# Optimization experiments

Measured on AMD Instinct MI355X. Metric: run time of the kernel, lower is better.

The kernel has to match this reference:

```python
import jax, jax.numpy as jnp
import numpy as np

N_NODES = 10000
N_EDGES = 320000
D_IN = 128
D_HID = 256
D_OUT = 128


def setup_inputs() -> dict:
    key = jax.random.key(0)
    k = jax.random.split(key, 6)
    idx_i = jax.random.randint(k[0], (N_EDGES,), 0, N_NODES)
    idx_j = jax.random.randint(k[1], (N_EDGES,), 0, N_NODES)
    prop = jax.random.normal(k[2], (N_NODES, D_IN), dtype=jnp.float32)
    basis = jax.random.normal(k[3], (N_EDGES, D_IN), dtype=jnp.float32)
    W1 = jax.random.normal(k[4], (D_IN, D_HID), dtype=jnp.float32) * (1.0 / np.sqrt(D_IN))
    b1 = jnp.zeros((D_HID,), dtype=jnp.float32)
    W2 = jax.random.normal(k[5], (D_HID, D_OUT), dtype=jnp.float32) * (1.0 / np.sqrt(D_HID))
    b2 = jnp.zeros((D_OUT,), dtype=jnp.float32)
    return {"idx_i": idx_i, "idx_j": idx_j, "prop": prop, "basis": basis,
            "W1": W1, "b1": b1, "W2": W2, "b2": b2}


def reference(idx_i, idx_j, prop, basis, W1, b1, W2, b2):
    # gather node features to edges, combine with basis: [E, D_IN]
    inter = prop[idx_i] + basis + prop[idx_j]
    # MLP: Linear(128->256) + tanh, then Linear(256->128) (no final activation)
    h = jnp.tanh(inter @ W1 + b1)  # [E, D_HID]
    out = h @ W2 + b2              # [E, D_OUT]
    return out
```

## Files before the change

kernel.cpp:

```cpp
#include <hip/hip_runtime.h>


#define N_EDGES 320000
#define DI 128
#define DH 256
#define DO 128
#define TM 64
#define NT_TILES (N_EDGES / TM)
#define PERSIST_GRID 768

typedef _Float16 half8v __attribute__((ext_vector_type(8)));
typedef _Float16 half4v __attribute__((ext_vector_type(4)));
typedef float floatx16 __attribute__((ext_vector_type(16)));

__device__ __forceinline__ float fast_tanh(float x) {
    float ax = __builtin_fabsf(x);
    float e = __expf(2.0f * ax);
    float t = 1.0f - 2.0f * __builtin_amdgcn_rcpf(e + 1.0f);
    return __builtin_copysignf(t, x);
}

#define BAR() do { asm volatile("s_waitcnt lgkmcnt(0)" ::: "memory"); \
                   __builtin_amdgcn_s_barrier();                      \
                   asm volatile("" ::: "memory"); } while (0)

__global__ __launch_bounds__(256) void wconvert(
    const float* __restrict__ W1, const float* __restrict__ W2,
    _Float16* __restrict__ W1T, _Float16* __restrict__ W2T)
{
    __shared__ float sT[32][33];
    int b = blockIdx.x;
    const float* src; _Float16* dst; int R, C, r0, c0;
    if (b < 32) { src = W1; dst = W1T; R = DI;  C = DH; r0 = (b & 3) * 32;  c0 = (b >> 2) * 32; }
    else { b -= 32; src = W2; dst = W2T; R = DH; C = DO; r0 = (b & 7) * 32; c0 = (b >> 3) * 32; }

    const int tid = threadIdx.x;
    const int cc = tid & 31, rr = tid >> 5;
    #pragma unroll
    for (int p = 0; p < 4; ++p) {
        int r = rr + p * 8;
        sT[r][cc] = src[(size_t)(r0 + r) * C + c0 + cc];
    }
    __syncthreads();
    #pragma unroll
    for (int p = 0; p < 4; ++p) {
        int c = rr + p * 8;
        dst[(size_t)(c0 + c) * R + r0 + cc] = (_Float16)sT[cc][c];
    }
}

__global__ __launch_bounds__(256, 2) void pilayer_main(
    const int* __restrict__ idx_i, const int* __restrict__ idx_j,
    const float* __restrict__ prop, const float* __restrict__ basis,
    const _Float16* __restrict__ W1T, const float* __restrict__ b1,
    const _Float16* __restrict__ W2T, const float* __restrict__ b2,
    float* __restrict__ out)
{
    __shared__ _Float16 sA[TM][DI + 8];
    __shared__ _Float16 sH[TM][DH + 8];

    const int tid = threadIdx.x;
    const int w   = tid >> 6;
    const int l   = tid & 63;
    const int lm  = l & 31;
    const int lk  = (l >> 5) * 8;
    const int rowq = 4 * (l >> 5);
    const int c4  = (tid & 31) * 4;
    const int r0  = tid >> 5;

    int t = blockIdx.x;

    {
        #pragma unroll
        for (int p = 0; p < 8; ++p) {
            const int r = r0 + p * 8;
            const int e = t * TM + r;
            const int ii = idx_i[e], jj = idx_j[e];
            const float4 a  = *(const float4*)(prop  + (size_t)ii * DI + c4);
            const float4 bv = *(const float4*)(prop  + (size_t)jj * DI + c4);
            const float4 c  = *(const float4*)(basis + (size_t)e  * DI + c4);
            half4v hv;
            hv[0] = (_Float16)(a.x + bv.x + c.x);
            hv[1] = (_Float16)(a.y + bv.y + c.y);
            hv[2] = (_Float16)(a.z + bv.z + c.z);
            hv[3] = (_Float16)(a.w + bv.w + c.w);
            *(half4v*)(&sA[r][c4]) = hv;
        }
    }
    BAR();

    for (; t < NT_TILES; t += PERSIST_GRID) {
        const int tn = t + PERSIST_GRID;
        const bool pf = (tn < NT_TILES);

        int ii[8], jj[8];
        float4 gc[8];
        if (pf) {
            #pragma unroll
            for (int p = 0; p < 8; ++p) {
                const int e = tn * TM + r0 + p * 8;
                ii[p] = idx_i[e];
                jj[p] = idx_j[e];
                gc[p] = *(const float4*)(basis + (size_t)e * DI + c4);
            }
        }

        floatx16 hacc[2][2] = {};
        {
            const _Float16* w1p = W1T + (size_t)(w * 64 + lm) * DI + lk;
            __builtin_amdgcn_s_setprio(1);
            #pragma unroll 4
            for (int kt = 0; kt < 8; ++kt) {
                const int ko = kt * 16;
                half8v a0  = *(const half8v*)(&sA[lm][ko + lk]);
                half8v a1  = *(const half8v*)(&sA[32 + lm][ko + lk]);
                half8v b0  = *(const half8v*)(w1p + ko);
                half8v b1f = *(const half8v*)(w1p + 32 * DI + ko);
                hacc[0][0] = __builtin_amdgcn_mfma_f32_32x32x16_f16(a0, b0,  hacc[0][0], 0, 0, 0);
                hacc[1][0] = __builtin_amdgcn_mfma_f32_32x32x16_f16(a1, b0,  hacc[1][0], 0, 0, 0);
                hacc[0][1] = __builtin_amdgcn_mfma_f32_32x32x16_f16(a0, b1f, hacc[0][1], 0, 0, 0);
                hacc[1][1] = __builtin_amdgcn_mfma_f32_32x32x16_f16(a1, b1f, hacc[1][1], 0, 0, 0);
            }
            __builtin_amdgcn_s_setprio(0);
        }

        float4 ga[8], gb[8];
        if (pf) {
            #pragma unroll
            for (int p = 0; p < 8; ++p) {
                ga[p] = *(const float4*)(prop + (size_t)ii[p] * DI + c4);
                gb[p] = *(const float4*)(prop + (size_t)jj[p] * DI + c4);
            }
        }

        {
            const float bias0 = b1[w * 64 + lm];
            const float bias1 = b1[w * 64 + 32 + lm];
            #pragma unroll
            for (int mt = 0; mt < 2; ++mt) {
                #pragma unroll
                for (int r = 0; r < 16; ++r) {
                    const int row = mt * 32 + (r & 3) + 8 * (r >> 2) + rowq;
                    sH[row][w * 64 + lm]      = (_Float16)fast_tanh(hacc[mt][0][r] + bias0);
                    sH[row][w * 64 + 32 + lm] = (_Float16)fast_tanh(hacc[mt][1][r] + bias1);
                }
            }
        }
        BAR();

        floatx16 oacc[2] = {};
        {
            const _Float16* w2p = W2T + (size_t)(w * 32 + lm) * DH + lk;
            __builtin_amdgcn_s_setprio(1);
            #pragma unroll 4
            for (int kt = 0; kt < 16; ++kt) {
                const int ko = kt * 16;
                half8v a0 = *(const half8v*)(&sH[lm][ko + lk]);
                half8v a1 = *(const half8v*)(&sH[32 + lm][ko + lk]);
                half8v bb = *(const half8v*)(w2p + ko);
                oacc[0] = __builtin_amdgcn_mfma_f32_32x32x16_f16(a0, bb, oacc[0], 0, 0, 0);
                oacc[1] = __builtin_amdgcn_mfma_f32_32x32x16_f16(a1, bb, oacc[1], 0, 0, 0);
            }
            __builtin_amdgcn_s_setprio(0);
        }

        if (pf) {
            #pragma unroll
            for (int p = 0; p < 8; ++p) {
                const int r = r0 + p * 8;
                half4v hv;
                hv[0] = (_Float16)(ga[p].x + gb[p].x + gc[p].x);
                hv[1] = (_Float16)(ga[p].y + gb[p].y + gc[p].y);
                hv[2] = (_Float16)(ga[p].z + gb[p].z + gc[p].z);
                hv[3] = (_Float16)(ga[p].w + gb[p].w + gc[p].w);
                *(half4v*)(&sA[r][c4]) = hv;
            }
        }

        {
            const int col = w * 32 + lm;
            const float bias = b2[col];
            #pragma unroll
            for (int mt = 0; mt < 2; ++mt) {
                #pragma unroll
                for (int r = 0; r < 16; ++r) {
                    const int row = t * TM + mt * 32 + (r & 3) + 8 * (r >> 2) + rowq;
                    __builtin_nontemporal_store(oacc[mt][r] + bias,
                                                out + (size_t)row * DO + col);
                }
            }
        }

        BAR();
    }
}

extern "C" void kernel_launch(void* const* d_in, const int* in_sizes, int n_in,
                              void* d_out, int out_size, void* d_ws, size_t ws_size,
                              hipStream_t stream) {
    const int*   idx_i = (const int*)d_in[0];
    const int*   idx_j = (const int*)d_in[1];
    const float* prop  = (const float*)d_in[2];
    const float* basis = (const float*)d_in[3];
    const float* W1    = (const float*)d_in[4];
    const float* b1    = (const float*)d_in[5];
    const float* W2    = (const float*)d_in[6];
    const float* b2    = (const float*)d_in[7];
    float* out = (float*)d_out;

    _Float16* W1T = (_Float16*)d_ws;
    _Float16* W2T = W1T + (size_t)DI * DH;

    wconvert<<<64, 256, 0, stream>>>(W1, W2, W1T, W2T);
    pilayer_main<<<PERSIST_GRID, 256, 0, stream>>>(idx_i, idx_j, prop, basis,
                                                   W1T, b1, W2T, b2, out);
}
```

Before: 399.6 us.

## Precompute per-node prop@W1 and gather projected features instead of raw props

```diff
diff --git a/kernel.cpp b/kernel.cpp
--- a/kernel.cpp
+++ b/kernel.cpp
@@ -2,27 +2,21 @@
 
 
 #define N_EDGES 320000
+#define N_NODES 10000
 #define DI 128
 #define DH 256
 #define DO 128
 #define TM 64
-#define NT_TILES (N_EDGES / TM)
-#define PERSIST_GRID 768
+#define NBLK (N_EDGES / TM)
 
 typedef _Float16 half8v __attribute__((ext_vector_type(8)));
 typedef _Float16 half4v __attribute__((ext_vector_type(4)));
 typedef float floatx16 __attribute__((ext_vector_type(16)));
 
 __device__ __forceinline__ float fast_tanh(float x) {
-    float ax = __builtin_fabsf(x);
-    float e = __expf(2.0f * ax);
-    float t = 1.0f - 2.0f * __builtin_amdgcn_rcpf(e + 1.0f);
-    return __builtin_copysignf(t, x);
-}
-
-#define BAR() do { asm volatile("s_waitcnt lgkmcnt(0)" ::: "memory"); \
-                   __builtin_amdgcn_s_barrier();                      \
-                   asm volatile("" ::: "memory"); } while (0)
+    float e = __expf(2.0f * x);
+    return 1.0f - 2.0f * __builtin_amdgcn_rcpf(e + 1.0f);
+}
 
 __global__ __launch_bounds__(256) void wconvert(
     const float* __restrict__ W1, const float* __restrict__ W2,
@@ -49,149 +43,170 @@
     }
 }
 
-__global__ __launch_bounds__(256, 2) void pilayer_main(
+__global__ __launch_bounds__(256) void p1comp(
+    const float* __restrict__ prop, const _Float16* __restrict__ W1T,
+    float* __restrict__ P1)
+{
+    __shared__ _Float16 sHi[TM][DI + 8];
+    __shared__ _Float16 sLo[TM][DI + 8];
+
+    const int tid = threadIdx.x;
+    const int e0  = blockIdx.x * TM;
+    const int c4  = (tid & 31) * 4;
+    const int r0  = tid >> 5;
+
+    #pragma unroll
+    for (int p = 0; p < 8; ++p) {
+        const int r = r0 + p * 8;
+        int n = e0 + r; if (n > N_NODES - 1) n = N_NODES - 1;
+        const float4 a = *(const float4*)(prop + (size_t)n * DI + c4);
+        half4v hi, lo;
+        hi[0] = (_Float16)a.x; lo[0] = (_Float16)(a.x - (float)hi[0]);
+        hi[1] = (_Float16)a.y; lo[1] = (_Float16)(a.y - (float)hi[1]);
+        hi[2] = (_Float16)a.z; lo[2] = (_Float16)(a.z - (float)hi[2]);
+        hi[3] = (_Float16)a.w; lo[3] = (_Float16)(a.w - (float)hi[3]);
+        *(half4v*)(&sHi[r][c4]) = hi;
+        *(half4v*)(&sLo[r][c4]) = lo;
+    }
+    __syncthreads();
+
+    const int w  = tid >> 6, l = tid & 63;
+    const int lm = l & 31, lk = (l >> 5) * 8, rowq = 4 * (l >> 5);
+
+    floatx16 acc[2][2] = {};
+    const _Float16* w1p = W1T + (size_t)(w * 64 + lm) * DI + lk;
+    #pragma unroll 2
+    for (int kt = 0; kt < 8; ++kt) {
+        const int ko = kt * 16;
+        half8v b0  = *(const half8v*)(w1p + ko);
+        half8v b1f = *(const half8v*)(w1p + 32 * DI + ko);
+        half8v h0  = *(const half8v*)(&sHi[lm][ko + lk]);
+        half8v h1  = *(const half8v*)(&sHi[32 + lm][ko + lk]);
+        half8v l0  = *(const half8v*)(&sLo[lm][ko + lk]);
+        half8v l1  = *(const half8v*)(&sLo[32 + lm][ko + lk]);
+        acc[0][0] = __builtin_amdgcn_mfma_f32_32x32x16_f16(h0, b0,  acc[0][0], 0, 0, 0);
+        acc[0][0] = __builtin_amdgcn_mfma_f32_32x32x16_f16(l0, b0,  acc[0][0], 0, 0, 0);
+        acc[1][0] = __builtin_amdgcn_mfma_f32_32x32x16_f16(h1, b0,  acc[1][0], 0, 0, 0);
+        acc[1][0] = __builtin_amdgcn_mfma_f32_32x32x16_f16(l1, b0,  acc[1][0], 0, 0, 0);
+        acc[0][1] = __builtin_amdgcn_mfma_f32_32x32x16_f16(h0, b1f, acc[0][1], 0, 0, 0);
+        acc[0][1] = __builtin_amdgcn_mfma_f32_32x32x16_f16(l0, b1f, acc[0][1], 0, 0, 0);
+        acc[1][1] = __builtin_amdgcn_mfma_f32_32x32x16_f16(h1, b1f, acc[1][1], 0, 0, 0);
+        acc[1][1] = __builtin_amdgcn_mfma_f32_32x32x16_f16(l1, b1f, acc[1][1], 0, 0, 0);
+    }
+
+    #pragma unroll
+    for (int mt = 0; mt < 2; ++mt) {
+        #pragma unroll
+        for (int r = 0; r < 16; ++r) {
+            const int row = e0 + mt * 32 + (r & 3) + 8 * (r >> 2) + rowq;
+            if (row < N_NODES) {
+                P1[(size_t)row * DH + w * 64 + lm]      = acc[mt][0][r];
+                P1[(size_t)row * DH + w * 64 + 32 + lm] = acc[mt][1][r];
+            }
+        }
+    }
+}
+
+__global__ __launch_bounds__(256) void pilayer_main(
     const int* __restrict__ idx_i, const int* __restrict__ idx_j,
-    const float* __restrict__ prop, const float* __restrict__ basis,
+    const float* __restrict__ basis, const float* __restrict__ P1,
     const _Float16* __restrict__ W1T, const float* __restrict__ b1,
     const _Float16* __restrict__ W2T, const float* __restrict__ b2,
     float* __restrict__ out)
 {
     __shared__ _Float16 sA[TM][DI + 8];
     __shared__ _Float16 sH[TM][DH + 8];
+    __shared__ int2 sIdx[TM];
 
     const int tid = threadIdx.x;
-    const int w   = tid >> 6;
-    const int l   = tid & 63;
-    const int lm  = l & 31;
-    const int lk  = (l >> 5) * 8;
-    const int rowq = 4 * (l >> 5);
+    const int e0  = blockIdx.x * TM;
     const int c4  = (tid & 31) * 4;
     const int r0  = tid >> 5;
 
-    int t = blockIdx.x;
-
-    {
+    #pragma unroll
+    for (int p = 0; p < 8; ++p) {
+        const int r = r0 + p * 8;
+        const float4 c = *(const float4*)(basis + (size_t)(e0 + r) * DI + c4);
+        half4v hv;
+        hv[0] = (_Float16)c.x; hv[1] = (_Float16)c.y;
+        hv[2] = (_Float16)c.z; hv[3] = (_Float16)c.w;
+        *(half4v*)(&sA[r][c4]) = hv;
+    }
+    if (tid < TM) sIdx[tid] = make_int2(idx_i[e0 + tid], idx_j[e0 + tid]);
+    __syncthreads();
+
+    const int w  = tid >> 6, l = tid & 63;
+    const int lm = l & 31, lk = (l >> 5) * 8, rowq = 4 * (l >> 5);
+
+    floatx16 hacc[2][2] = {};
+    {
+        const _Float16* w1p = W1T + (size_t)(w * 64 + lm) * DI + lk;
+        __builtin_amdgcn_s_setprio(1);
+        #pragma unroll 4
+        for (int kt = 0; kt < 8; ++kt) {
+            const int ko = kt * 16;
+            half8v a0  = *(const half8v*)(&sA[lm][ko + lk]);
+            half8v a1  = *(const half8v*)(&sA[32 + lm][ko + lk]);
+            half8v b0  = *(const half8v*)(w1p + ko);
+            half8v b1f = *(const half8v*)(w1p + 32 * DI + ko);
+            hacc[0][0] = __builtin_amdgcn_mfma_f32_32x32x16_f16(a0, b0,  hacc[0][0], 0, 0, 0);
+            hacc[1][0] = __builtin_amdgcn_mfma_f32_32x32x16_f16(a1, b0,  hacc[1][0], 0, 0, 0);
+            hacc[0][1] = __builtin_amdgcn_mfma_f32_32x32x16_f16(a0, b1f, hacc[0][1], 0, 0, 0);
+            hacc[1][1] = __builtin_amdgcn_mfma_f32_32x32x16_f16(a1, b1f, hacc[1][1], 0, 0, 0);
+        }
+        __builtin_amdgcn_s_setprio(0);
+    }
+
+    {
+        const float bias0 = b1[w * 64 + lm];
+        const float bias1 = b1[w * 64 + 32 + lm];
+        const float* p1c0 = P1 + (w * 64 + lm);
+        const float* p1c1 = P1 + (w * 64 + 32 + lm);
         #pragma unroll
-        for (int p = 0; p < 8; ++p) {
-            const int r = r0 + p * 8;
-            const int e = t * TM + r;
-            const int ii = idx_i[e], jj = idx_j[e];
-            const float4 a  = *(const float4*)(prop  + (size_t)ii * DI + c4);
-            const float4 bv = *(const float4*)(prop  + (size_t)jj * DI + c4);
-            const float4 c  = *(const float4*)(basis + (size_t)e  * DI + c4);
-            half4v hv;
-            hv[0] = (_Float16)(a.x + bv.x + c.x);
-            hv[1] = (_Float16)(a.y + bv.y + c.y);
-            hv[2] = (_Float16)(a.z + bv.z + c.z);
-            hv[3] = (_Float16)(a.w + bv.w + c.w);
-            *(half4v*)(&sA[r][c4]) = hv;
-        }
-    }
-    BAR();
-
-    for (; t < NT_TILES; t += PERSIST_GRID) {
-        const int tn = t + PERSIST_GRID;
-        const bool pf = (tn < NT_TILES);
-
-        int ii[8], jj[8];
-        float4 gc[8];
-        if (pf) {
+        for (int mt = 0; mt < 2; ++mt) {
             #pragma unroll
-            for (int p = 0; p < 8; ++p) {
-                const int e = tn * TM + r0 + p * 8;
-                ii[p] = idx_i[e];
-                jj[p] = idx_j[e];
-                gc[p] = *(const float4*)(basis + (size_t)e * DI + c4);
+            for (int r = 0; r < 16; ++r) {
+                const int rl = mt * 32 + (r & 3) + 8 * (r >> 2) + rowq;
+                const int2 ij = sIdx[rl];
+                const size_t oi = (size_t)ij.x * DH;
+                const size_t oj = (size_t)ij.y * DH;
+                const float v0 = hacc[mt][0][r] + bias0 + p1c0[oi] + p1c0[oj];
+                const float v1 = hacc[mt][1][r] + bias1 + p1c1[oi] + p1c1[oj];
+                sH[rl][w * 64 + lm]      = (_Float16)fast_tanh(v0);
+                sH[rl][w * 64 + 32 + lm] = (_Float16)fast_tanh(v1);
             }
         }
-
-        floatx16 hacc[2][2] = {};
-        {
-            const _Float16* w1p = W1T + (size_t)(w * 64 + lm) * DI + lk;
-            __builtin_amdgcn_s_setprio(1);
-            #pragma unroll 4
-            for (int kt = 0; kt < 8; ++kt) {
-                const int ko = kt * 16;
-                half8v a0  = *(const half8v*)(&sA[lm][ko + lk]);
-                half8v a1  = *(const half8v*)(&sA[32 + lm][ko + lk]);
-                half8v b0  = *(const half8v*)(w1p + ko);
-                half8v b1f = *(const half8v*)(w1p + 32 * DI + ko);
-                hacc[0][0] = __builtin_amdgcn_mfma_f32_32x32x16_f16(a0, b0,  hacc[0][0], 0, 0, 0);
-                hacc[1][0] = __builtin_amdgcn_mfma_f32_32x32x16_f16(a1, b0,  hacc[1][0], 0, 0, 0);
-                hacc[0][1] = __builtin_amdgcn_mfma_f32_32x32x16_f16(a0, b1f, hacc[0][1], 0, 0, 0);
-                hacc[1][1] = __builtin_amdgcn_mfma_f32_32x32x16_f16(a1, b1f, hacc[1][1], 0, 0, 0);
+    }
+    __syncthreads();
+
+    floatx16 oacc[2] = {};
+    {
+        const _Float16* w2p = W2T + (size_t)(w * 32 + lm) * DH + lk;
+        __builtin_amdgcn_s_setprio(1);
+        #pragma unroll 4
+        for (int kt = 0; kt < 16; ++kt) {
+            const int ko = kt * 16;
+            half8v a0 = *(const half8v*)(&sH[lm][ko + lk]);
+            half8v a1 = *(const half8v*)(&sH[32 + lm][ko + lk]);
+            half8v bb = *(const half8v*)(w2p + ko);
+            oacc[0] = __builtin_amdgcn_mfma_f32_32x32x16_f16(a0, bb, oacc[0], 0, 0, 0);
+            oacc[1] = __builtin_amdgcn_mfma_f32_32x32x16_f16(a1, bb, oacc[1], 0, 0, 0);
+        }
+        __builtin_amdgcn_s_setprio(0);
+    }
+
+    {
+        const int col = w * 32 + lm;
+        const float bias = b2[col];
+        #pragma unroll
+        for (int mt = 0; mt < 2; ++mt) {
+            #pragma unroll
+            for (int r = 0; r < 16; ++r) {
+                const int row = e0 + mt * 32 + (r & 3) + 8 * (r >> 2) + rowq;
+                __builtin_nontemporal_store(oacc[mt][r] + bias,
+                                            out + (size_t)row * DO + col);
             }
-            __builtin_amdgcn_s_setprio(0);
-        }
-
-        float4 ga[8], gb[8];
-        if (pf) {
-            #pragma unroll
-            for (int p = 0; p < 8; ++p) {
-                ga[p] = *(const float4*)(prop + (size_t)ii[p] * DI + c4);
-                gb[p] = *(const float4*)(prop + (size_t)jj[p] * DI + c4);
-            }
-        }
-
-        {
-            const float bias0 = b1[w * 64 + lm];
-            const float bias1 = b1[w * 64 + 32 + lm];
-            #pragma unroll
-            for (int mt = 0; mt < 2; ++mt) {
-                #pragma unroll
-                for (int r = 0; r < 16; ++r) {
-                    const int row = mt * 32 + (r & 3) + 8 * (r >> 2) + rowq;
-                    sH[row][w * 64 + lm]      = (_Float16)fast_tanh(hacc[mt][0][r] + bias0);
-                    sH[row][w * 64 + 32 + lm] = (_Float16)fast_tanh(hacc[mt][1][r] + bias1);
-                }
-            }
-        }
-        BAR();
-
-        floatx16 oacc[2] = {};
-        {
-            const _Float16* w2p = W2T + (size_t)(w * 32 + lm) * DH + lk;
-            __builtin_amdgcn_s_setprio(1);
-            #pragma unroll 4
-            for (int kt = 0; kt < 16; ++kt) {
-                const int ko = kt * 16;
-                half8v a0 = *(const half8v*)(&sH[lm][ko + lk]);
-                half8v a1 = *(const half8v*)(&sH[32 + lm][ko + lk]);
-                half8v bb = *(const half8v*)(w2p + ko);
-                oacc[0] = __builtin_amdgcn_mfma_f32_32x32x16_f16(a0, bb, oacc[0], 0, 0, 0);
-                oacc[1] = __builtin_amdgcn_mfma_f32_32x32x16_f16(a1, bb, oacc[1], 0, 0, 0);
-            }
-            __builtin_amdgcn_s_setprio(0);
-        }
-
-        if (pf) {
-            #pragma unroll
-            for (int p = 0; p < 8; ++p) {
-                const int r = r0 + p * 8;
-                half4v hv;
-                hv[0] = (_Float16)(ga[p].x + gb[p].x + gc[p].x);
-                hv[1] = (_Float16)(ga[p].y + gb[p].y + gc[p].y);
-                hv[2] = (_Float16)(ga[p].z + gb[p].z + gc[p].z);
-                hv[3] = (_Float16)(ga[p].w + gb[p].w + gc[p].w);
-                *(half4v*)(&sA[r][c4]) = hv;
-            }
-        }
-
-        {
-            const int col = w * 32 + lm;
-            const float bias = b2[col];
-            #pragma unroll
-            for (int mt = 0; mt < 2; ++mt) {
-                #pragma unroll
-                for (int r = 0; r < 16; ++r) {
-                    const int row = t * TM + mt * 32 + (r & 3) + 8 * (r >> 2) + rowq;
-                    __builtin_nontemporal_store(oacc[mt][r] + bias,
-                                                out + (size_t)row * DO + col);
-                }
-            }
-        }
-
-        BAR();
+        }
     }
 }
 
@@ -210,8 +225,10 @@
 
     _Float16* W1T = (_Float16*)d_ws;
     _Float16* W2T = W1T + (size_t)DI * DH;
+    float*    P1  = (float*)((char*)d_ws + 128 * 1024);
 
     wconvert<<<64, 256, 0, stream>>>(W1, W2, W1T, W2T);
-    pilayer_main<<<PERSIST_GRID, 256, 0, stream>>>(idx_i, idx_j, prop, basis,
-                                                   W1T, b1, W2T, b2, out);
-}
+    p1comp<<<(N_NODES + TM - 1) / TM, 256, 0, stream>>>(prop, W1T, P1);
+    pilayer_main<<<NBLK, 256, 0, stream>>>(idx_i, idx_j, basis, P1,
+                                           W1T, b1, W2T, b2, out);
+}
```

Result: no change. 403.8 us (+1.1%).
